# Optimization experiments

Hardware: AMD Instinct MI355X
Metric: run time of the kernel (lower is better)

The kernel has to match this reference:

```python
import jax, jax.numpy as jnp
import numpy as np
import math

B, NH, DIM = 8, 12, 768
NP, NF = 196, 16            # n (patches per frame), num_frames
DH = DIM // NH              # 64
D3 = 3 * DH                 # per-head feature dim after projection (192)
SEQ = NP * NF               # 3136 body tokens (+1 cls)
ROT = DH                    # rotary dim (RotaryEmbedding(dim=64))
SCALE = 1.0 / (math.sqrt(DH) * NH)


def _heads(t):
    b, s, _ = t.shape
    return t.reshape(b, s, NH, D3).transpose(0, 2, 1, 3)  # b h s d


def _rope(x):
    # lucidrains-style interleaved rotary on the first ROT dims of each head
    s = x.shape[2]
    inv_freq = 1.0 / (10000.0 ** (jnp.arange(0, ROT, 2, dtype=jnp.float32) / ROT))
    freqs = jnp.arange(s, dtype=jnp.float32)[:, None] * inv_freq  # [s, ROT/2]
    freqs = jnp.repeat(freqs, 2, axis=-1)                          # [s, ROT]
    cos, sin = jnp.cos(freqs), jnp.sin(freqs)
    xr, xp = x[..., :ROT], x[..., ROT:]
    x1, x2 = xr[..., ::2], xr[..., 1::2]
    half = jnp.stack((-x2, x1), axis=-1).reshape(xr.shape)
    return jnp.concatenate([xr * cos + half * sin, xp], axis=-1)


def _att_sum(q, k, v):
    # softmax(q k^T * SCALE) v, then sum over queries keepdim (dim 2)
    p = jax.nn.softmax(jnp.einsum('bhqd,bhkd->bhqk', q, k) * SCALE, axis=-1)
    return jnp.einsum('bhqk,bhkd->bhqd', p, v).sum(axis=2, keepdims=True)


def setup_inputs():
    key = jax.random.key(0)
    ks = jax.random.split(key, 11)
    p = lambda k, sh: jax.random.normal(k, sh, jnp.float32) * 0.02
    return {
        'x': jax.random.normal(ks[0], (B, SEQ + 1, DIM), jnp.float32),
        'Wq': p(ks[1], (DIM, 3 * DIM)), 'bq': p(ks[2], (3 * DIM,)),
        'Wk': p(ks[3], (DIM, 3 * DIM)), 'bk': p(ks[4], (3 * DIM,)),
        'Wv': p(ks[5], (DIM, 3 * DIM)), 'bv': p(ks[6], (3 * DIM,)),
        'Wt': p(ks[7], (3 * DIM, DIM)), 'bt': p(ks[8], (DIM,)),
        'Wf': p(ks[9], (3 * DIM, DIM)), 'bf': p(ks[10], (DIM,)),
    }


def reference(x, Wq, bq, Wk, bk, Wv, bv, Wt, bt, Wf, bf):
    body = x[:, 1:, :]
    # NOTE: the original swaps k/v projections for body tokens (k_mat uses self.v, v_mat uses self.k)
    q = _rope(_heads(body @ Wq + bq))
    k = _rope(_heads(body @ Wv + bv))
    v = _heads(body @ Wk + bk)

    # cls-token attention over the full sequence (correct k/v mapping here)
    q_cls = _heads(x[:, 0:1, :] @ Wq + bq)          # [b,h,1,d]
    k_cls = _heads(x @ Wk + bk)
    v_cls = _heads(x @ Wv + bv)
    p_cls = jax.nn.softmax(jnp.einsum('bhqd,bhkd->bhqk', q_cls, k_cls) * SCALE, axis=-1)
    cls_out = jnp.einsum('bhqk,bhkd->bhqd', p_cls, v_cls)  # [b,h,1,d]

    # temporal attention per spatial position x = 1..NP-1, vectorized
    # token index t = f*NP + x  ->  reshape [b,h,NF,NP,d], move spatial first
    qg = q.reshape(B, NH, NF, NP, D3).transpose(0, 1, 3, 2, 4)[:, :, 1:]  # [b,h,NP-1,NF,d]
    kg = k.reshape(B, NH, NF, NP, D3).transpose(0, 1, 3, 2, 4)[:, :, 1:]
    vg = v.reshape(B, NH, NF, NP, D3).transpose(0, 1, 3, 2, 4)[:, :, 1:]
    pg = jax.nn.softmax(jnp.einsum('bhxfd,bhxgd->bhxfg', qg, kg) * SCALE, axis=-1)
    tmp = jnp.einsum('bhxfg,bhxgd->bhxfd', pg, vg).sum(axis=3)  # sum over query frames -> [b,h,NP-1,d]

    temporal = jnp.tile(tmp, (1, 1, NF, 1))  # torch .repeat tiles -> [b,h,(NP-1)*NF,d]
    ti = temporal.transpose(0, 2, 1, 3).reshape(B, (NP - 1) * NF, NH * D3) @ Wt + bt

    # second pass (q uses self.q, v uses self.k, k uses self.v per original)
    q2 = _heads(ti @ Wq + bq)
    v2 = _heads(ti @ Wk + bk)
    k2 = _heads(ti @ Wv + bv)
    outs = [_att_sum(q2[:, :, 0:NP], k2[:, :, 0:NP], v2[:, :, 0:NP])]
    for xi in range(1, NF):  # small fixed loop over frames
        outs.append(_att_sum(q2[:, :, xi:xi + NP], k2[:, :, xi::NP], v2[:, :, xi::NP]))
    t2 = jnp.concatenate(outs, axis=2)        # [b,h,NF,d]
    t2 = jnp.tile(t2, (1, 1, NP, 1))          # [b,h,SEQ,d]
    t2 = jnp.concatenate([cls_out, t2], axis=2)  # [b,h,SEQ+1,d]
    return t2.transpose(0, 2, 1, 3).reshape(B, SEQ + 1, NH * D3) @ Wf + bf
```

## Files before the change

kernel.cpp:

```cpp
#include <hip/hip_runtime.h>
#include <cstdint>
#include <cstddef>


typedef unsigned short u16;
typedef __attribute__((ext_vector_type(8))) short short8;
typedef __attribute__((ext_vector_type(4))) float f32x4;

#define DEV static __device__ __forceinline__
#define AS1 __attribute__((address_space(1)))
#define AS3 __attribute__((address_space(3)))

DEV float b2f(u16 u) { union { unsigned int i; float f; } v; v.i = ((unsigned int)u) << 16; return v.f; }
DEV float b2fs(short s) { return b2f((u16)s); }
DEV u16 f2b(float f) {
    union { float f; unsigned int i; } v; v.f = f;
    unsigned int r = v.i + 0x7fffu + ((v.i >> 16) & 1u);
    return (u16)(r >> 16);
}
DEV void gld16(const u16* g, u16* l) {
    __builtin_amdgcn_global_load_lds((AS1 void*)(g), (AS3 void*)(l), 16, 0, 0);
}

constexpr int   ROWS  = 3137;
constexpr int   NPm1  = 195;
constexpr int   MT    = 8 * NPm1;
constexpr int   N3    = 2304;
constexpr float SCALE = 1.0f / 96.0f;
constexpr size_t P2Z  = (size_t)MT * N3;
constexpr int   CLS_NS = 32;
constexpr int   CLS_RS = 99;
constexpr int   LDK   = 200;

DEV float wave_max(float v) {
#pragma unroll
    for (int off = 32; off; off >>= 1) v = fmaxf(v, __shfl_xor(v, off));
    return v;
}
DEV float wave_sum(float v) {
#pragma unroll
    for (int off = 32; off; off >>= 1) v += __shfl_xor(v, off);
    return v;
}
DEV float block_max256(float v, float* red) {
    v = wave_max(v);
    __syncthreads();
    if ((threadIdx.x & 63) == 0) red[threadIdx.x >> 6] = v;
    __syncthreads();
    return fmaxf(fmaxf(red[0], red[1]), fmaxf(red[2], red[3]));
}
DEV float block_sum256(float v, float* red) {
    v = wave_sum(v);
    __syncthreads();
    if ((threadIdx.x & 63) == 0) red[threadIdx.x >> 6] = v;
    __syncthreads();
    return (red[0] + red[1]) + (red[2] + red[3]);
}

__global__ __launch_bounds__(256) void detect_dtype(const u16* __restrict__ x,
                                                    int* __restrict__ flag) {
    __shared__ int cnt;
    if (threadIdx.x == 0) cnt = 0;
    __syncthreads();
    int c = 0;
    for (int i = threadIdx.x; i < 8192; i += 256) {
        unsigned e = (x[i] >> 7) & 0xFFu;
        if (e >= 134u) c++;
    }
#pragma unroll
    for (int off = 32; off; off >>= 1) c += __shfl_xor(c, off);
    if ((threadIdx.x & 63) == 0) atomicAdd(&cnt, c);
    __syncthreads();
    if (threadIdx.x == 0) *flag = (cnt > 16) ? 1 : 0;
}

__global__ __launch_bounds__(256) void convert_x(const void* __restrict__ x,
                                                 u16* __restrict__ xb,
                                                 const int* __restrict__ dflag) {
    const int fl = *dflag;
    int t = blockIdx.x * 256 + threadIdx.x;
    size_t e0 = (size_t)t * 8;
    if (fl) {
        const float* p = (const float*)x + e0;
        float4 u0 = *(const float4*)p, u1 = *(const float4*)(p + 4);
        short8 r;
        r[0]=(short)f2b(u0.x); r[1]=(short)f2b(u0.y); r[2]=(short)f2b(u0.z); r[3]=(short)f2b(u0.w);
        r[4]=(short)f2b(u1.x); r[5]=(short)f2b(u1.y); r[6]=(short)f2b(u1.z); r[7]=(short)f2b(u1.w);
        *(short8*)(xb + e0) = r;
    } else {
        *(short8*)(xb + e0) = *(const short8*)((const u16*)x + e0);
    }
}

__global__ __launch_bounds__(256) void transpose_k(const void* __restrict__ in,
                                                   u16* __restrict__ out, int R, int C,
                                                   const int* __restrict__ dflag) {
    const int fl = *dflag;
    __shared__ u16 t[32][33];
    int bx = blockIdx.x * 32, by = blockIdx.y * 32;
    int tx = threadIdx.x & 31, ty = threadIdx.x >> 5;
#pragma unroll
    for (int i = 0; i < 32; i += 8) {
        int r = by + ty + i, c = bx + tx;
        if (r < R && c < C) {
            size_t idx = (size_t)r * C + c;
            t[ty + i][tx] = fl ? f2b(((const float*)in)[idx]) : ((const u16*)in)[idx];
        }
    }
    __syncthreads();
#pragma unroll
    for (int i = 0; i < 32; i += 8) {
        int c = bx + ty + i, r = by + tx;
        if (c < C && r < R) out[(size_t)c * R + r] = t[tx][ty + i];
    }
}

__global__ __launch_bounds__(256) void rope_tab_k(float* __restrict__ tab) {
    int t = blockIdx.x * 256 + threadIdx.x;
    if (t >= 3136 * 32) return;
    int s = t >> 5, i = t & 31;
    float inv = powf(10000.0f, -(float)(2 * i) * (1.0f / 64.0f));
    float sn, cs;
    sincosf((float)s * inv, &sn, &cs);
    tab[t * 2]     = cs;
    tab[t * 2 + 1] = sn;
}

DEV short8 pack_f32x8(const float* p) {
    const float4 u0 = *(const float4*)p;
    const float4 u1 = *(const float4*)(p + 4);
    short8 r;
    r[0]=(short)f2b(u0.x); r[1]=(short)f2b(u0.y); r[2]=(short)f2b(u0.z); r[3]=(short)f2b(u0.w);
    r[4]=(short)f2b(u1.x); r[5]=(short)f2b(u1.y); r[6]=(short)f2b(u1.z); r[7]=(short)f2b(u1.w);
    return r;
}

__global__ __launch_bounds__(256) void gemm_bt(const void* __restrict__ A, size_t aoff,
                                               const u16* __restrict__ BT,
                                               const void* __restrict__ b0p,
                                               const void* __restrict__ b1p,
                                               const void* __restrict__ b2p,
                                               void* __restrict__ C,
                                               int M, int N, int K,
                                               const int* __restrict__ dflag,
                                               int araw, int cf32) {
    const int fl = *dflag;
    const int af32 = araw && fl;
    const int z = blockIdx.z;
    const u16* Bz = BT + (size_t)z * N * K;
    const void* bias = (z == 0) ? b0p : (z == 1) ? b1p : b2p;

    __shared__ u16 As[128 * 32];
    __shared__ u16 Bs[128 * 32];

    const int tid  = threadIdx.x;
    const int lane = tid & 63;
    const int wave = tid >> 6;
    const int wm   = wave & 1;
    const int wn   = wave >> 1;
    const int quad = lane >> 4;
    const int l16  = lane & 15;

    const int m0 = blockIdx.y * 128;
    const int n0 = blockIdx.x * 128;

    f32x4 acc[4][4] = {};

    if (!af32) {
        const u16* Ab = (const u16*)A + aoff;
        int srow = wave * 32 + (lane >> 2);
        int scol = (lane & 3) * 8;
        int ar0 = m0 + srow;      if (ar0 > M - 1) ar0 = M - 1;
        int ar1 = m0 + srow + 16; if (ar1 > M - 1) ar1 = M - 1;
        const u16* gA0 = Ab + (size_t)ar0 * K + scol;
        const u16* gA1 = Ab + (size_t)ar1 * K + scol;
        const u16* gB0 = Bz + (size_t)(n0 + srow) * K + scol;
        const u16* gB1 = Bz + (size_t)(n0 + srow + 16) * K + scol;
        u16* lA0 = As + wave * 1024;
        u16* lA1 = As + wave * 1024 + 512;
        u16* lB0 = Bs + wave * 1024;
        u16* lB1 = Bs + wave * 1024 + 512;

        for (int k0 = 0; k0 < K; k0 += 32) {
            __syncthreads();
            gld16(gA0 + k0, lA0);
            gld16(gA1 + k0, lA1);
            gld16(gB0 + k0, lB0);
            gld16(gB1 + k0, lB1);
            __syncthreads();

            short8 af[4], bfr[4];
#pragma unroll
            for (int i = 0; i < 4; i++)
                af[i] = *(const short8*)(&As[(wm * 64 + i * 16 + l16) * 32 + quad * 8]);
#pragma unroll
            for (int j = 0; j < 4; j++)
                bfr[j] = *(const short8*)(&Bs[(wn * 64 + j * 16 + l16) * 32 + quad * 8]);
#pragma unroll
            for (int i = 0; i < 4; i++)
#pragma unroll
                for (int j = 0; j < 4; j++)
                    acc[i][j] = __builtin_amdgcn_mfma_f32_16x16x32_bf16(af[i], bfr[j], acc[i][j], 0, 0, 0);
        }
    } else {
        const int r0 = tid >> 2;
        const int kp = (tid & 3) << 3;
        int ga0 = m0 + r0;       if (ga0 > M - 1) ga0 = M - 1;
        int ga1 = m0 + r0 + 64;  if (ga1 > M - 1) ga1 = M - 1;
        const size_t arow0 = aoff + (size_t)ga0 * K + kp;
        const size_t arow1 = aoff + (size_t)ga1 * K + kp;
        const u16* Bp0 = Bz + (size_t)(n0 + r0) * K + kp;
        const u16* Bp1 = Bz + (size_t)(n0 + r0 + 64) * K + kp;

        for (int k0 = 0; k0 < K; k0 += 32) {
            short8 a0 = pack_f32x8((const float*)A + arow0 + k0);
            short8 a1 = pack_f32x8((const float*)A + arow1 + k0);
            short8 bv0 = *(const short8*)(Bp0 + k0);
            short8 bv1 = *(const short8*)(Bp1 + k0);
            __syncthreads();
            *(short8*)(&As[r0 * 32 + kp])        = a0;
            *(short8*)(&As[(r0 + 64) * 32 + kp]) = a1;
            *(short8*)(&Bs[r0 * 32 + kp])        = bv0;
            *(short8*)(&Bs[(r0 + 64) * 32 + kp]) = bv1;
            __syncthreads();

            short8 af[4], bfr[4];
#pragma unroll
            for (int i = 0; i < 4; i++)
                af[i] = *(const short8*)(&As[(wm * 64 + i * 16 + l16) * 32 + quad * 8]);
#pragma unroll
            for (int j = 0; j < 4; j++)
                bfr[j] = *(const short8*)(&Bs[(wn * 64 + j * 16 + l16) * 32 + quad * 8]);
#pragma unroll
            for (int i = 0; i < 4; i++)
#pragma unroll
                for (int j = 0; j < 4; j++)
                    acc[i][j] = __builtin_amdgcn_mfma_f32_16x16x32_bf16(af[i], bfr[j], acc[i][j], 0, 0, 0);
        }
    }

#pragma unroll
    for (int j = 0; j < 4; j++) {
        int col = n0 + wn * 64 + j * 16 + l16;
        float bb = fl ? ((const float*)bias)[col] : b2f(((const u16*)bias)[col]);
#pragma unroll
        for (int i = 0; i < 4; i++) {
            int rowb = m0 + wm * 64 + i * 16 + quad * 4;
#pragma unroll
            for (int r = 0; r < 4; r++) {
                int row = rowb + r;
                if (row < M) {
                    size_t idx = (size_t)z * M * N + (size_t)row * N + col;
                    float v = acc[i][j][r] + bb;
                    if (cf32) ((float*)C)[idx] = v;
                    else      ((u16*)C)[idx]  = f2b(v);
                }
            }
        }
    }
}

__global__ __launch_bounds__(256) void cls_part(const u16* __restrict__ Pb, size_t PZv,
                                                float* __restrict__ part, int b0) {
    int h = blockIdx.x, sp = blockIdx.y, bl = blockIdx.z;
    int b = b0 + bl;
    int base = sp * CLS_RS;
    int cnt = ROWS - base; if (cnt > CLS_RS) cnt = CLS_RS;
    __shared__ u16 Ksh[CLS_RS * LDK];
    __shared__ float qs[192];
    __shared__ float sc[CLS_RS];
    __shared__ float red[4];
    int tid = threadIdx.x;
    const size_t hbase = (size_t)bl * ROWS * N3 + (size_t)h * 192;
    const u16* Pq  = Pb;
    const u16* Pkc = Pb + PZv;
    const u16* Pvc = Pb + 2 * PZv;

    if (tid < 192) qs[tid] = b2f(Pq[hbase + tid]);
    for (int i = tid; i < cnt * 24; i += 256) {
        int r = i / 24, c = (i % 24) * 8;
        *(short8*)&Ksh[r * LDK + c] =
            *(const short8*)(Pkc + hbase + (size_t)(base + r) * N3 + c);
    }
    __syncthreads();

    float sval = -1e30f;
    if (tid < cnt) {
        float s = 0.f;
#pragma unroll
        for (int c = 0; c < 24; c++) {
            short8 v8 = *(const short8*)&Ksh[tid * LDK + c * 8];
#pragma unroll
            for (int j = 0; j < 8; j++) s += qs[c * 8 + j] * b2fs(v8[j]);
        }
        sval = s * SCALE;
    }
    float m = block_max256(sval, red);
    float e = (tid < cnt) ? __expf(sval - m) : 0.f;
    float l = block_sum256(e, red);
    if (tid < cnt) sc[tid] = e;
    __syncthreads();

    float* pp = part + ((size_t)(b * 12 + h) * CLS_NS + sp) * 194;
    if (tid == 0) { pp[0] = m; pp[1] = l; }
    if (tid < 192) {
        float acc = 0.f;
        const u16* vb = Pvc + hbase + tid;
        for (int r = 0; r < cnt; r++) acc += sc[r] * b2f(vb[(size_t)(base + r) * N3]);
        pp[2 + tid] = acc;
    }
}

__global__ __launch_bounds__(192) void cls_merge(const float* __restrict__ part,
                                                 u16* __restrict__ Fmat) {
    int h = blockIdx.x, b = blockIdx.y;
    int tid = threadIdx.x;
    const float* p0 = part + (size_t)(b * 12 + h) * CLS_NS * 194;
    float M = -1e30f;
#pragma unroll
    for (int s = 0; s < CLS_NS; s++) M = fmaxf(M, p0[s * 194]);
    float L = 0.f, acc = 0.f;
#pragma unroll
    for (int s = 0; s < CLS_NS; s++) {
        float w = __expf(p0[s * 194] - M);
        L += w * p0[s * 194 + 1];
        acc += w * p0[s * 194 + 2 + tid];
    }
    Fmat[(size_t)(b * 17) * N3 + (size_t)h * 192 + tid] = f2b(acc / L);
}

__global__ __launch_bounds__(128) void temporal_attn(const u16* __restrict__ Pb, size_t PZv,
                                                     const float* __restrict__ tab,
                                                     u16* __restrict__ tmp, int b0) {
    int p = blockIdx.x + 1, h = blockIdx.y, bl = blockIdx.z;
    int b = b0 + bl;
    __shared__ u16 Qs[16 * LDK];
    __shared__ u16 Ks[16 * LDK];
    __shared__ u16 Vs[16 * LDK];
    __shared__ float w[16];
    int tid = threadIdx.x;
    const u16* Pq = Pb;
    const u16* Pk = Pb + 2 * PZv;
    const u16* Pv = Pb + PZv;
    const size_t rbase = (size_t)bl * ROWS;

    for (int i = tid; i < 384; i += 128) {
        int f = i / 24, c = (i % 24) * 8;
        int s = f * 196 + p;
        size_t gidx = (rbase + 1 + s) * N3 + (size_t)h * 192 + c;
        short8 q8 = *(const short8*)(Pq + gidx);
        short8 k8 = *(const short8*)(Pk + gidx);
        short8 v8 = *(const short8*)(Pv + gidx);
        if (c < 64) {
            const float* tp = tab + ((size_t)s * 32 + (c >> 1)) * 2;
            float4 t0 = *(const float4*)tp;
            float4 t1 = *(const float4*)(tp + 4);
            float cs[4] = {t0.x, t0.z, t1.x, t1.z};
            float sn[4] = {t0.y, t0.w, t1.y, t1.w};
            short8 qo, ko;
#pragma unroll
            for (int j = 0; j < 4; j++) {
                float q1 = b2fs(q8[2 * j]), q2 = b2fs(q8[2 * j + 1]);
                float k1 = b2fs(k8[2 * j]), k2 = b2fs(k8[2 * j + 1]);
                qo[2 * j]     = (short)f2b(q1 * cs[j] - q2 * sn[j]);
                qo[2 * j + 1] = (short)f2b(q2 * cs[j] + q1 * sn[j]);
                ko[2 * j]     = (short)f2b(k1 * cs[j] - k2 * sn[j]);
                ko[2 * j + 1] = (short)f2b(k2 * cs[j] + k1 * sn[j]);
            }
            q8 = qo; k8 = ko;
        }
        *(short8*)&Qs[f * LDK + c] = q8;
        *(short8*)&Ks[f * LDK + c] = k8;
        *(short8*)&Vs[f * LDK + c] = v8;
    }
    __syncthreads();

    if (tid < 64) {
        int quad = tid >> 4, l16 = tid & 15;
        short8 Af[6], Bf[6];
#pragma unroll
        for (int ks = 0; ks < 6; ks++) {
            Af[ks] = *(const short8*)&Qs[l16 * LDK + quad * 8 + ks * 32];
            Bf[ks] = *(const short8*)&Ks[l16 * LDK + quad * 8 + ks * 32];
        }
        f32x4 S = {0.f, 0.f, 0.f, 0.f};
#pragma unroll
        for (int ks = 0; ks < 6; ks++)
            S = __builtin_amdgcn_mfma_f32_16x16x32_bf16(Af[ks], Bf[ks], S, 0, 0, 0);
        float wcol = 0.f;
#pragma unroll
        for (int r = 0; r < 4; r++) {
            float v = S[r] * SCALE;
            float m = v;
#pragma unroll
            for (int k = 1; k < 16; k <<= 1) m = fmaxf(m, __shfl_xor(m, k));
            float e = __expf(v - m);
            float l = e;
#pragma unroll
            for (int k = 1; k < 16; k <<= 1) l += __shfl_xor(l, k);
            wcol += e / l;
        }
        wcol += __shfl_xor(wcol, 16);
        wcol += __shfl_xor(wcol, 32);
        if (quad == 0) w[l16] = wcol;
    }
    __syncthreads();

    for (int d = tid; d < 192; d += 128) {
        float acc = 0.f;
#pragma unroll
        for (int g = 0; g < 16; g++) acc += w[g] * b2f(Vs[g * LDK + d]);
        tmp[(size_t)(b * NPm1 + p - 1) * N3 + (size_t)h * 192 + d] = f2b(acc);
    }
}

__global__ __launch_bounds__(256) void wacc_zero(float* __restrict__ wacc) {
    wacc[blockIdx.x * 256 + threadIdx.x] = 0.f;
}

__global__ __launch_bounds__(256) void attn2_sc(const u16* __restrict__ P2,
                                                float* __restrict__ wacc) {
    int t = blockIdx.x, h = blockIdx.y, b = blockIdx.z;
    __shared__ u16 Ks[195 * LDK];
    __shared__ u16 Qs[31 * LDK];
    __shared__ float pm[4][16], ps[4][16];
    int tid = threadIdx.x;
    const size_t hb = (size_t)b * NPm1 * N3 + (size_t)h * 192;
    const u16* Q  = P2;
    const u16* Kc = P2 + 2 * P2Z;

    for (int i = tid; i < 195 * 24; i += 256) {
        int r = i / 24, c = (i % 24) * 8;
        *(short8*)&Ks[r * LDK + c] = *(const short8*)(Kc + hb + (size_t)r * N3 + c);
    }
    for (int i = tid; i < 31 * 24; i += 256) {
        int r = i / 24, c = (i % 24) * 8;
        int qr = (t * 16 + r) % 195;
        *(short8*)&Qs[r * LDK + c] = *(const short8*)(Q + hb + (size_t)qr * N3 + c);
    }
    __syncthreads();

    int wave = tid >> 6, lane = tid & 63, quad = lane >> 4, l16 = lane & 15;
    float* wb = wacc + (size_t)((b * 12 + h) * 16) * 196;

    for (int xi = 1 + wave; xi <= 15; xi += 4) {
        short8 Af[6], Bf[6];
#pragma unroll
        for (int ks = 0; ks < 6; ks++) {
            Af[ks] = *(const short8*)&Qs[(xi + l16) * LDK + quad * 8 + ks * 32];
            Bf[ks] = *(const short8*)&Ks[(xi + l16) * LDK + quad * 8 + ks * 32];
        }
        f32x4 S = {0.f, 0.f, 0.f, 0.f};
#pragma unroll
        for (int ks = 0; ks < 6; ks++)
            S = __builtin_amdgcn_mfma_f32_16x16x32_bf16(Af[ks], Bf[ks], S, 0, 0, 0);
        float wcol = 0.f;
#pragma unroll
        for (int r = 0; r < 4; r++) {
            float v = S[r] * SCALE;
            float m = v;
#pragma unroll
            for (int k = 1; k < 16; k <<= 1) m = fmaxf(m, __shfl_xor(m, k));
            float e = __expf(v - m);
            float l = e;
#pragma unroll
            for (int k = 1; k < 16; k <<= 1) l += __shfl_xor(l, k);
            bool qok = (t * 16 + quad * 4 + r) <= 195;
            wcol += qok ? e / l : 0.f;
        }
        wcol += __shfl_xor(wcol, 16);
        wcol += __shfl_xor(wcol, 32);
        if (quad == 0) atomicAdd(&wb[xi * 196 + l16], wcol);
    }

    short8 Af0[6];
#pragma unroll
    for (int ks = 0; ks < 6; ks++)
        Af0[ks] = *(const short8*)&Qs[l16 * LDK + quad * 8 + ks * 32];

    f32x4 Sc[4];
    int   cl[4];
    int   cn = 0;
    for (int c = wave; c < 13; c += 4) {
        int g = c * 16 + l16;
        int krow = g % 195;
        short8 Bf[6];
#pragma unroll
        for (int ks = 0; ks < 6; ks++)
            Bf[ks] = *(const short8*)&Ks[krow * LDK + quad * 8 + ks * 32];
        f32x4 S = {0.f, 0.f, 0.f, 0.f};
#pragma unroll
        for (int ks = 0; ks < 6; ks++)
            S = __builtin_amdgcn_mfma_f32_16x16x32_bf16(Af0[ks], Bf[ks], S, 0, 0, 0);
        bool kbad = g > 195;
#pragma unroll
        for (int r = 0; r < 4; r++) S[r] = kbad ? -1e30f : S[r] * SCALE;
        Sc[cn] = S; cl[cn] = c; cn++;
    }
#pragma unroll
    for (int r = 0; r < 4; r++) {
        float v = -1e30f;
        for (int n = 0; n < cn; n++) v = fmaxf(v, Sc[n][r]);
#pragma unroll
        for (int k = 1; k < 16; k <<= 1) v = fmaxf(v, __shfl_xor(v, k));
        if (l16 == 0) pm[wave][quad * 4 + r] = v;
    }
    __syncthreads();
    float gmx[4], tot[4];
#pragma unroll
    for (int r = 0; r < 4; r++) {
        int qr = quad * 4 + r;
        gmx[r] = fmaxf(fmaxf(pm[0][qr], pm[1][qr]), fmaxf(pm[2][qr], pm[3][qr]));
    }
#pragma unroll
    for (int r = 0; r < 4; r++) {
        float s = 0.f;
        for (int n = 0; n < cn; n++) {
            float e = __expf(Sc[n][r] - gmx[r]);
            Sc[n][r] = e;
            s += e;
        }
#pragma unroll
        for (int k = 1; k < 16; k <<= 1) s += __shfl_xor(s, k);
        if (l16 == 0) ps[wave][quad * 4 + r] = s;
    }
    __syncthreads();
#pragma unroll
    for (int r = 0; r < 4; r++) {
        int qr = quad * 4 + r;
        tot[r] = (ps[0][qr] + ps[1][qr]) + (ps[2][qr] + ps[3][qr]);
    }
    for (int n = 0; n < cn; n++) {
        float wv = 0.f;
#pragma unroll
        for (int r = 0; r < 4; r++) {
            bool qok = (t * 16 + quad * 4 + r) <= 195;
            wv += qok ? Sc[n][r] / tot[r] : 0.f;
        }
        wv += __shfl_xor(wv, 16);
        wv += __shfl_xor(wv, 32);
        int g = cl[n] * 16 + l16;
        if (quad == 0 && g <= 195) atomicAdd(&wb[g], wv);
    }
}

__global__ __launch_bounds__(192) void attn2_fin(const u16* __restrict__ P2,
                                                 const float* __restrict__ wacc,
                                                 u16* __restrict__ Fmat) {
    int xi = blockIdx.x, h = blockIdx.y, b = blockIdx.z;
    int Nk = (xi == 0) ? 196 : 16;
    int tid = threadIdx.x;
    const u16* V = P2 + P2Z;
    const size_t hb = (size_t)b * NPm1 * N3 + (size_t)h * 192;
    const float* wb = wacc + (size_t)((b * 12 + h) * 16 + xi) * 196;
    float acc = 0.f;
    for (int g = 0; g < Nk; g++) {
        int kr = (xi == 0) ? (g % 195) : (xi + g);
        acc += wb[g] * b2f(V[hb + (size_t)kr * N3 + tid]);
    }
    Fmat[(size_t)(b * 17 + 1 + xi) * N3 + (size_t)h * 192 + tid] = f2b(acc);
}

__global__ __launch_bounds__(256) void scatter_out(const float* __restrict__ F17,
                                                   void* __restrict__ out,
                                                   const int* __restrict__ dflag) {
    const int fl = *dflag;
    int t = blockIdx.x * 256 + threadIdx.x;
    int c = t % 96;
    int rem = t / 96;
    int s = rem % ROWS;
    int b = rem / ROWS;
    int src = b * 17 + (s == 0 ? 0 : 1 + ((s - 1) & 15));
    const float* sp = F17 + ((size_t)src * 96 + c) * 8;
    if (fl) {
        float* o = (float*)out + (size_t)t * 8;
        *(float4*)o       = *(const float4*)sp;
        *(float4*)(o + 4) = *(const float4*)(sp + 4);
    } else {
        u16* o = (u16*)out + (size_t)t * 8;
        short8 v;
#pragma unroll
        for (int j = 0; j < 8; j++) v[j] = (short)f2b(sp[j]);
        *(short8*)o = v;
    }
}

extern "C" void kernel_launch(void* const* d_in, const int* in_sizes, int n_in,
                              void* d_out, int out_size, void* d_ws, size_t ws_size,
                              hipStream_t stream) {
    const void* x   = d_in[0];
    const void* Wq  = d_in[1];
    const void* bq  = d_in[2];
    const void* Wk  = d_in[3];
    const void* bk  = d_in[4];
    const void* Wv  = d_in[5];
    const void* bv  = d_in[6];
    const void* Wt  = d_in[7];
    const void* bt  = d_in[8];
    const void* Wf  = d_in[9];
    const void* bfb = d_in[10];
    (void)in_sizes; (void)n_in; (void)out_size;

    auto al = [](size_t b) { return (b + 255) & ~(size_t)255; };
    const size_t szFlag = al(256);
    const size_t szWT   = al((size_t)3 * N3 * 768 * 2);
    const size_t szTmp  = al((size_t)MT * N3 * 2);
    const size_t szFmat = al((size_t)136 * N3 * 2);
    const size_t szRope = al((size_t)3136 * 32 * 2 * 4);
    const size_t szClsP = al((size_t)8 * 12 * CLS_NS * 194 * 4);
    const size_t szWacc = al((size_t)96 * 16 * 196 * 4);
    const size_t szXb   = al((size_t)8 * ROWS * 768 * 2);
    const size_t szB    = al(3 * P2Z * 2) + al((size_t)MT * 768 * 2) +
                          al((size_t)768 * N3 * 2) * 2 + al((size_t)136 * 768 * 4);
    const size_t basePerst = szFlag + szWT + szTmp + szFmat + szRope + szClsP + szWacc;

    int bs = 1; int usexb = 0;
    {
        const int cand[4] = {8, 4, 2, 1};
        for (int i = 0; i < 4; i++) {
            size_t szP = al((size_t)3 * cand[i] * ROWS * N3 * 2);
            size_t need = basePerst + szXb + (szP > szB ? szP : szB);
            if (ws_size >= need) { bs = cand[i]; usexb = 1; break; }
        }
        if (!usexb) {
            size_t szP = al((size_t)3 * ROWS * N3 * 2);
            size_t need = basePerst + (szP > szB ? szP : szB);
            if (ws_size < need) return;
        }
    }

    char* ws = (char*)d_ws;
    size_t off = 0;
    auto allocB = [&](size_t bytes) { char* p = ws + off; off += al(bytes); return p; };
    int*   dflag = (int*)allocB(256);
    u16*   WT    = (u16*)allocB((size_t)3 * N3 * 768 * 2);
    u16*   tmp   = (u16*)allocB((size_t)MT * N3 * 2);
    u16*   Fmat  = (u16*)allocB((size_t)136 * N3 * 2);
    float* ropeT = (float*)allocB((size_t)3136 * 32 * 2 * 4);
    float* clsP  = (float*)allocB((size_t)8 * 12 * CLS_NS * 194 * 4);
    float* wacc  = (float*)allocB((size_t)96 * 16 * 196 * 4);
    u16*   xb    = usexb ? (u16*)allocB((size_t)8 * ROWS * 768 * 2) : nullptr;
    size_t aliasOff = off;
    u16* Pb = (u16*)allocB((size_t)3 * bs * ROWS * N3 * 2);
    off = aliasOff;
    u16*   P2  = (u16*)allocB(3 * P2Z * 2);
    u16*   tiu = (u16*)allocB((size_t)MT * 768 * 2);
    u16*   WtT = (u16*)allocB((size_t)768 * N3 * 2);
    u16*   WfT = (u16*)allocB((size_t)768 * N3 * 2);
    float* F17 = (float*)allocB((size_t)136 * 768 * 4);

    const size_t PZv = (size_t)bs * ROWS * N3;

    detect_dtype<<<dim3(1), 256, 0, stream>>>((const u16*)x, dflag);
    rope_tab_k<<<dim3(392), 256, 0, stream>>>(ropeT);
    if (usexb) convert_x<<<dim3(9411), 256, 0, stream>>>(x, xb, dflag);

    transpose_k<<<dim3(72, 24), 256, 0, stream>>>(Wq, WT, 768, N3, dflag);
    transpose_k<<<dim3(72, 24), 256, 0, stream>>>(Wk, WT + (size_t)N3 * 768, 768, N3, dflag);
    transpose_k<<<dim3(72, 24), 256, 0, stream>>>(Wv, WT + (size_t)2 * N3 * 768, 768, N3, dflag);

    for (int b0 = 0; b0 < 8; b0 += bs) {
        int Mv = bs * ROWS;
        size_t aoff = (size_t)b0 * ROWS * 768;
        if (usexb)
            gemm_bt<<<dim3(18, (Mv + 127) / 128, 3), 256, 0, stream>>>(
                xb, aoff, WT, bq, bk, bv, Pb, Mv, N3, 768, dflag, 0, 0);
        else
            gemm_bt<<<dim3(18, (Mv + 127) / 128, 3), 256, 0, stream>>>(
                x, aoff, WT, bq, bk, bv, Pb, Mv, N3, 768, dflag, 1, 0);
        cls_part<<<dim3(12, CLS_NS, bs), 256, 0, stream>>>(Pb, PZv, clsP, b0);
        temporal_attn<<<dim3(195, 12, bs), 128, 0, stream>>>(Pb, PZv, ropeT, tmp, b0);
    }
    cls_merge<<<dim3(12, 8), 192, 0, stream>>>(clsP, Fmat);

    transpose_k<<<dim3(24, 72), 256, 0, stream>>>(Wt, WtT, N3, 768, dflag);
    transpose_k<<<dim3(24, 72), 256, 0, stream>>>(Wf, WfT, N3, 768, dflag);

    gemm_bt<<<dim3(6, 13, 1), 256, 0, stream>>>(tmp, 0, WtT, bt, bt, bt, tiu,
                                                MT, 768, N3, dflag, 0, 0);
    gemm_bt<<<dim3(18, 13, 3), 256, 0, stream>>>(tiu, 0, WT, bq, bk, bv, P2,
                                                 MT, N3, 768, dflag, 0, 0);

    wacc_zero<<<dim3(1176), 256, 0, stream>>>(wacc);
    attn2_sc<<<dim3(13, 12, 8), 256, 0, stream>>>(P2, wacc);
    attn2_fin<<<dim3(16, 12, 8), 192, 0, stream>>>(P2, wacc, Fmat);

    gemm_bt<<<dim3(6, 2, 1), 256, 0, stream>>>(Fmat, 0, WfT, bfb, bfb, bfb, F17,
                                               136, 768, N3, dflag, 0, 1);

    scatter_out<<<dim3(9411), 256, 0, stream>>>(F17, d_out, dflag);
}
```

Before: 1.180 ms.

## Merge prep, attention and finalize kernels to cut launch count

Folds the dtype detection, weight transposes, input conversion, wacc zeroing and rope table into one prep kernel. Each kernel now recomputes the dtype flag per wave instead of reading a stored flag. Fuses cls_part with temporal_attn and cls_merge with attn2_fin so fewer launches and serial dependencies remain. WtT/WfT move out of the aliased region so they can be transposed up front, which costs extra workspace, and the dtype check now samples fewer elements.

```diff
diff --git a/kernel.cpp b/kernel.cpp
--- a/kernel.cpp
+++ b/kernel.cpp
@@ -20,6 +20,17 @@
 }
 DEV void gld16(const u16* g, u16* l) {
     __builtin_amdgcn_global_load_lds((AS1 void*)(g), (AS3 void*)(l), 16, 0, 0);
+}
+
+DEV int detect_fl(const u16* x) {
+    int lane = threadIdx.x & 63;
+    const u16* p = x + lane * 8;
+    int c = 0;
+#pragma unroll
+    for (int j = 0; j < 8; j++) c += (((p[j] >> 7) & 0xFFu) >= 134u);
+#pragma unroll
+    for (int off = 32; off; off >>= 1) c += __shfl_xor(c, off);
+    return c > 8;
 }
 
 constexpr int   ROWS  = 3137;
@@ -57,73 +68,86 @@
     return (red[0] + red[1]) + (red[2] + red[3]);
 }
 
-__global__ __launch_bounds__(256) void detect_dtype(const u16* __restrict__ x,
-                                                    int* __restrict__ flag) {
-    __shared__ int cnt;
-    if (threadIdx.x == 0) cnt = 0;
-    __syncthreads();
-    int c = 0;
-    for (int i = threadIdx.x; i < 8192; i += 256) {
-        unsigned e = (x[i] >> 7) & 0xFFu;
-        if (e >= 134u) c++;
-    }
-#pragma unroll
-    for (int off = 32; off; off >>= 1) c += __shfl_xor(c, off);
-    if ((threadIdx.x & 63) == 0) atomicAdd(&cnt, c);
-    __syncthreads();
-    if (threadIdx.x == 0) *flag = (cnt > 16) ? 1 : 0;
-}
-
-__global__ __launch_bounds__(256) void convert_x(const void* __restrict__ x,
-                                                 u16* __restrict__ xb,
-                                                 const int* __restrict__ dflag) {
-    const int fl = *dflag;
-    int t = blockIdx.x * 256 + threadIdx.x;
-    size_t e0 = (size_t)t * 8;
-    if (fl) {
-        const float* p = (const float*)x + e0;
-        float4 u0 = *(const float4*)p, u1 = *(const float4*)(p + 4);
-        short8 r;
-        r[0]=(short)f2b(u0.x); r[1]=(short)f2b(u0.y); r[2]=(short)f2b(u0.z); r[3]=(short)f2b(u0.w);
-        r[4]=(short)f2b(u1.x); r[5]=(short)f2b(u1.y); r[6]=(short)f2b(u1.z); r[7]=(short)f2b(u1.w);
-        *(short8*)(xb + e0) = r;
-    } else {
-        *(short8*)(xb + e0) = *(const short8*)((const u16*)x + e0);
-    }
-}
-
-__global__ __launch_bounds__(256) void transpose_k(const void* __restrict__ in,
-                                                   u16* __restrict__ out, int R, int C,
-                                                   const int* __restrict__ dflag) {
-    const int fl = *dflag;
-    __shared__ u16 t[32][33];
-    int bx = blockIdx.x * 32, by = blockIdx.y * 32;
+DEV void do_transpose(const void* in, u16* out, int R, int C,
+                      int bx, int by, int fl, u16 (*tls)[33]) {
     int tx = threadIdx.x & 31, ty = threadIdx.x >> 5;
 #pragma unroll
     for (int i = 0; i < 32; i += 8) {
         int r = by + ty + i, c = bx + tx;
-        if (r < R && c < C) {
-            size_t idx = (size_t)r * C + c;
-            t[ty + i][tx] = fl ? f2b(((const float*)in)[idx]) : ((const u16*)in)[idx];
-        }
+        size_t idx = (size_t)r * C + c;
+        tls[ty + i][tx] = fl ? f2b(((const float*)in)[idx]) : ((const u16*)in)[idx];
     }
     __syncthreads();
 #pragma unroll
     for (int i = 0; i < 32; i += 8) {
         int c = bx + ty + i, r = by + tx;
-        if (c < C && r < R) out[(size_t)c * R + r] = t[tx][ty + i];
-    }
-}
-
-__global__ __launch_bounds__(256) void rope_tab_k(float* __restrict__ tab) {
-    int t = blockIdx.x * 256 + threadIdx.x;
-    if (t >= 3136 * 32) return;
-    int s = t >> 5, i = t & 31;
-    float inv = powf(10000.0f, -(float)(2 * i) * (1.0f / 64.0f));
-    float sn, cs;
-    sincosf((float)s * inv, &sn, &cs);
-    tab[t * 2]     = cs;
-    tab[t * 2 + 1] = sn;
+        out[(size_t)c * R + r] = tls[tx][ty + i];
+    }
+}
+
+__global__ __launch_bounds__(256) void prep(const u16* __restrict__ x,
+                                            const void* __restrict__ Wq,
+                                            const void* __restrict__ Wk,
+                                            const void* __restrict__ Wv,
+                                            const void* __restrict__ Wt,
+                                            const void* __restrict__ Wf,
+                                            u16* __restrict__ WT,
+                                            u16* __restrict__ WtT,
+                                            u16* __restrict__ WfT,
+                                            u16* __restrict__ xb,
+                                            float* __restrict__ wacc,
+                                            float* __restrict__ ropeT,
+                                            int usexb) {
+    __shared__ u16 tls[32][33];
+    int bid = blockIdx.x;
+    if (bid < 5184) {
+        int fl = detect_fl(x);
+        int z = bid / 1728, t = bid % 1728;
+        const void* W = (z == 0) ? Wq : (z == 1) ? Wk : Wv;
+        do_transpose(W, WT + (size_t)z * N3 * 768, 768, N3,
+                     (t % 72) * 32, (t / 72) * 32, fl, tls);
+        return;
+    }
+    bid -= 5184;
+    if (bid < 3456) {
+        int fl = detect_fl(x);
+        int z = bid / 1728, t = bid % 1728;
+        do_transpose(z ? Wf : Wt, z ? WfT : WtT, N3, 768,
+                     (t % 24) * 32, (t / 24) * 32, fl, tls);
+        return;
+    }
+    bid -= 3456;
+    if (bid < 9411) {
+        if (!usexb) return;
+        int fl = detect_fl(x);
+        size_t e0 = ((size_t)bid * 256 + threadIdx.x) * 8;
+        if (fl) {
+            const float* p = (const float*)x + e0;
+            float4 u0 = *(const float4*)p, u1 = *(const float4*)(p + 4);
+            short8 r;
+            r[0]=(short)f2b(u0.x); r[1]=(short)f2b(u0.y); r[2]=(short)f2b(u0.z); r[3]=(short)f2b(u0.w);
+            r[4]=(short)f2b(u1.x); r[5]=(short)f2b(u1.y); r[6]=(short)f2b(u1.z); r[7]=(short)f2b(u1.w);
+            *(short8*)(xb + e0) = r;
+        } else {
+            *(short8*)(xb + e0) = *(const short8*)(x + e0);
+        }
+        return;
+    }
+    bid -= 9411;
+    if (bid < 1176) {
+        wacc[(size_t)bid * 256 + threadIdx.x] = 0.f;
+        return;
+    }
+    bid -= 1176;
+    {
+        int t = bid * 256 + threadIdx.x;
+        int s = t >> 5, i = t & 31;
+        float inv = powf(10000.0f, -(float)(2 * i) * (1.0f / 64.0f));
+        float sn, cs;
+        sincosf((float)s * inv, &sn, &cs);
+        ropeT[t * 2]     = cs;
+        ropeT[t * 2 + 1] = sn;
+    }
 }
 
 DEV short8 pack_f32x8(const float* p) {
@@ -142,9 +166,9 @@
                                                const void* __restrict__ b2p,
                                                void* __restrict__ C,
                                                int M, int N, int K,
-                                               const int* __restrict__ dflag,
+                                               const u16* __restrict__ xdet,
                                                int araw, int cf32) {
-    const int fl = *dflag;
+    const int fl = detect_fl(xdet);
     const int af32 = araw && fl;
     const int z = blockIdx.z;
     const u16* Bz = BT + (size_t)z * N * K;
@@ -260,162 +284,141 @@
     }
 }
 
-__global__ __launch_bounds__(256) void cls_part(const u16* __restrict__ Pb, size_t PZv,
-                                                float* __restrict__ part, int b0) {
-    int h = blockIdx.x, sp = blockIdx.y, bl = blockIdx.z;
+__global__ __launch_bounds__(256) void phaseA_attn(const u16* __restrict__ Pb, size_t PZv,
+                                                   const float* __restrict__ tab,
+                                                   u16* __restrict__ tmp,
+                                                   float* __restrict__ clsP, int b0) {
+    __shared__ __align__(16) char smem[40800];
+    int xg = blockIdx.x, h = blockIdx.y, bl = blockIdx.z;
     int b = b0 + bl;
-    int base = sp * CLS_RS;
-    int cnt = ROWS - base; if (cnt > CLS_RS) cnt = CLS_RS;
-    __shared__ u16 Ksh[CLS_RS * LDK];
-    __shared__ float qs[192];
-    __shared__ float sc[CLS_RS];
-    __shared__ float red[4];
     int tid = threadIdx.x;
-    const size_t hbase = (size_t)bl * ROWS * N3 + (size_t)h * 192;
-    const u16* Pq  = Pb;
-    const u16* Pkc = Pb + PZv;
-    const u16* Pvc = Pb + 2 * PZv;
-
-    if (tid < 192) qs[tid] = b2f(Pq[hbase + tid]);
-    for (int i = tid; i < cnt * 24; i += 256) {
-        int r = i / 24, c = (i % 24) * 8;
-        *(short8*)&Ksh[r * LDK + c] =
-            *(const short8*)(Pkc + hbase + (size_t)(base + r) * N3 + c);
-    }
-    __syncthreads();
-
-    float sval = -1e30f;
-    if (tid < cnt) {
-        float s = 0.f;
-#pragma unroll
-        for (int c = 0; c < 24; c++) {
-            short8 v8 = *(const short8*)&Ksh[tid * LDK + c * 8];
-#pragma unroll
-            for (int j = 0; j < 8; j++) s += qs[c * 8 + j] * b2fs(v8[j]);
-        }
-        sval = s * SCALE;
-    }
-    float m = block_max256(sval, red);
-    float e = (tid < cnt) ? __expf(sval - m) : 0.f;
-    float l = block_sum256(e, red);
-    if (tid < cnt) sc[tid] = e;
-    __syncthreads();
-
-    float* pp = part + ((size_t)(b * 12 + h) * CLS_NS + sp) * 194;
-    if (tid == 0) { pp[0] = m; pp[1] = l; }
-    if (tid < 192) {
-        float acc = 0.f;
-        const u16* vb = Pvc + hbase + tid;
-        for (int r = 0; r < cnt; r++) acc += sc[r] * b2f(vb[(size_t)(base + r) * N3]);
-        pp[2 + tid] = acc;
-    }
-}
-
-__global__ __launch_bounds__(192) void cls_merge(const float* __restrict__ part,
-                                                 u16* __restrict__ Fmat) {
-    int h = blockIdx.x, b = blockIdx.y;
-    int tid = threadIdx.x;
-    const float* p0 = part + (size_t)(b * 12 + h) * CLS_NS * 194;
-    float M = -1e30f;
-#pragma unroll
-    for (int s = 0; s < CLS_NS; s++) M = fmaxf(M, p0[s * 194]);
-    float L = 0.f, acc = 0.f;
-#pragma unroll
-    for (int s = 0; s < CLS_NS; s++) {
-        float w = __expf(p0[s * 194] - M);
-        L += w * p0[s * 194 + 1];
-        acc += w * p0[s * 194 + 2 + tid];
-    }
-    Fmat[(size_t)(b * 17) * N3 + (size_t)h * 192 + tid] = f2b(acc / L);
-}
-
-__global__ __launch_bounds__(128) void temporal_attn(const u16* __restrict__ Pb, size_t PZv,
-                                                     const float* __restrict__ tab,
-                                                     u16* __restrict__ tmp, int b0) {
-    int p = blockIdx.x + 1, h = blockIdx.y, bl = blockIdx.z;
-    int b = b0 + bl;
-    __shared__ u16 Qs[16 * LDK];
-    __shared__ u16 Ks[16 * LDK];
-    __shared__ u16 Vs[16 * LDK];
-    __shared__ float w[16];
-    int tid = threadIdx.x;
-    const u16* Pq = Pb;
-    const u16* Pk = Pb + 2 * PZv;
-    const u16* Pv = Pb + PZv;
-    const size_t rbase = (size_t)bl * ROWS;
-
-    for (int i = tid; i < 384; i += 128) {
-        int f = i / 24, c = (i % 24) * 8;
-        int s = f * 196 + p;
-        size_t gidx = (rbase + 1 + s) * N3 + (size_t)h * 192 + c;
-        short8 q8 = *(const short8*)(Pq + gidx);
-        short8 k8 = *(const short8*)(Pk + gidx);
-        short8 v8 = *(const short8*)(Pv + gidx);
-        if (c < 64) {
-            const float* tp = tab + ((size_t)s * 32 + (c >> 1)) * 2;
-            float4 t0 = *(const float4*)tp;
-            float4 t1 = *(const float4*)(tp + 4);
-            float cs[4] = {t0.x, t0.z, t1.x, t1.z};
-            float sn[4] = {t0.y, t0.w, t1.y, t1.w};
-            short8 qo, ko;
-#pragma unroll
-            for (int j = 0; j < 4; j++) {
-                float q1 = b2fs(q8[2 * j]), q2 = b2fs(q8[2 * j + 1]);
-                float k1 = b2fs(k8[2 * j]), k2 = b2fs(k8[2 * j + 1]);
-                qo[2 * j]     = (short)f2b(q1 * cs[j] - q2 * sn[j]);
-                qo[2 * j + 1] = (short)f2b(q2 * cs[j] + q1 * sn[j]);
-                ko[2 * j]     = (short)f2b(k1 * cs[j] - k2 * sn[j]);
-                ko[2 * j + 1] = (short)f2b(k2 * cs[j] + k1 * sn[j]);
+
+    if (xg < 195) {
+        int p = xg + 1;
+        u16* Qs = (u16*)smem;
+        u16* Ks = Qs + 16 * LDK;
+        u16* Vs = Ks + 16 * LDK;
+        float* w = (float*)(smem + 3 * 16 * LDK * 2);
+        const u16* Pq = Pb;
+        const u16* Pk = Pb + 2 * PZv;
+        const u16* Pv = Pb + PZv;
+        const size_t rbase = (size_t)bl * ROWS;
+
+        for (int i = tid; i < 384; i += 256) {
+            int f = i / 24, c = (i % 24) * 8;
+            int s = f * 196 + p;
+            size_t gidx = (rbase + 1 + s) * N3 + (size_t)h * 192 + c;
+            short8 q8 = *(const short8*)(Pq + gidx);
+            short8 k8 = *(const short8*)(Pk + gidx);
+            short8 v8 = *(const short8*)(Pv + gidx);
+            if (c < 64) {
+                const float* tp = tab + ((size_t)s * 32 + (c >> 1)) * 2;
+                float4 t0 = *(const float4*)tp;
+                float4 t1 = *(const float4*)(tp + 4);
+                float cs[4] = {t0.x, t0.z, t1.x, t1.z};
+                float sn[4] = {t0.y, t0.w, t1.y, t1.w};
+                short8 qo, ko;
+#pragma unroll
+                for (int j = 0; j < 4; j++) {
+                    float q1 = b2fs(q8[2 * j]), q2 = b2fs(q8[2 * j + 1]);
+                    float k1 = b2fs(k8[2 * j]), k2 = b2fs(k8[2 * j + 1]);
+                    qo[2 * j]     = (short)f2b(q1 * cs[j] - q2 * sn[j]);
+                    qo[2 * j + 1] = (short)f2b(q2 * cs[j] + q1 * sn[j]);
+                    ko[2 * j]     = (short)f2b(k1 * cs[j] - k2 * sn[j]);
+                    ko[2 * j + 1] = (short)f2b(k2 * cs[j] + k1 * sn[j]);
+                }
+                q8 = qo; k8 = ko;
             }
-            q8 = qo; k8 = ko;
-        }
-        *(short8*)&Qs[f * LDK + c] = q8;
-        *(short8*)&Ks[f * LDK + c] = k8;
-        *(short8*)&Vs[f * LDK + c] = v8;
-    }
-    __syncthreads();
-
-    if (tid < 64) {
-        int quad = tid >> 4, l16 = tid & 15;
-        short8 Af[6], Bf[6];
-#pragma unroll
-        for (int ks = 0; ks < 6; ks++) {
-            Af[ks] = *(const short8*)&Qs[l16 * LDK + quad * 8 + ks * 32];
-            Bf[ks] = *(const short8*)&Ks[l16 * LDK + quad * 8 + ks * 32];
-        }
-        f32x4 S = {0.f, 0.f, 0.f, 0.f};
-#pragma unroll
-        for (int ks = 0; ks < 6; ks++)
-            S = __builtin_amdgcn_mfma_f32_16x16x32_bf16(Af[ks], Bf[ks], S, 0, 0, 0);
-        float wcol = 0.f;
-#pragma unroll
-        for (int r = 0; r < 4; r++) {
-            float v = S[r] * SCALE;
-            float m = v;
-#pragma unroll
-            for (int k = 1; k < 16; k <<= 1) m = fmaxf(m, __shfl_xor(m, k));
-            float e = __expf(v - m);
-            float l = e;
-#pragma unroll
-            for (int k = 1; k < 16; k <<= 1) l += __shfl_xor(l, k);
-            wcol += e / l;
-        }
-        wcol += __shfl_xor(wcol, 16);
-        wcol += __shfl_xor(wcol, 32);
-        if (quad == 0) w[l16] = wcol;
-    }
-    __syncthreads();
-
-    for (int d = tid; d < 192; d += 128) {
-        float acc = 0.f;
-#pragma unroll
-        for (int g = 0; g < 16; g++) acc += w[g] * b2f(Vs[g * LDK + d]);
-        tmp[(size_t)(b * NPm1 + p - 1) * N3 + (size_t)h * 192 + d] = f2b(acc);
-    }
-}
-
-__global__ __launch_bounds__(256) void wacc_zero(float* __restrict__ wacc) {
-    wacc[blockIdx.x * 256 + threadIdx.x] = 0.f;
+            *(short8*)&Qs[f * LDK + c] = q8;
+            *(short8*)&Ks[f * LDK + c] = k8;
+            *(short8*)&Vs[f * LDK + c] = v8;
+        }
+        __syncthreads();
+
+        if (tid < 64) {
+            int quad = tid >> 4, l16 = tid & 15;
+            short8 Af[6], Bf[6];
+#pragma unroll
+            for (int ks = 0; ks < 6; ks++) {
+                Af[ks] = *(const short8*)&Qs[l16 * LDK + quad * 8 + ks * 32];
+                Bf[ks] = *(const short8*)&Ks[l16 * LDK + quad * 8 + ks * 32];
+            }
+            f32x4 S = {0.f, 0.f, 0.f, 0.f};
+#pragma unroll
+            for (int ks = 0; ks < 6; ks++)
+                S = __builtin_amdgcn_mfma_f32_16x16x32_bf16(Af[ks], Bf[ks], S, 0, 0, 0);
+            float wcol = 0.f;
+#pragma unroll
+            for (int r = 0; r < 4; r++) {
+                float v = S[r] * SCALE;
+                float m = v;
+#pragma unroll
+                for (int k = 1; k < 16; k <<= 1) m = fmaxf(m, __shfl_xor(m, k));
+                float e = __expf(v - m);
+                float l = e;
+#pragma unroll
+                for (int k = 1; k < 16; k <<= 1) l += __shfl_xor(l, k);
+                wcol += e / l;
+            }
+            wcol += __shfl_xor(wcol, 16);
+            wcol += __shfl_xor(wcol, 32);
+            if (quad == 0) w[l16] = wcol;
+        }
+        __syncthreads();
+
+        if (tid < 192) {
+            float acc = 0.f;
+#pragma unroll
+            for (int g = 0; g < 16; g++) acc += w[g] * b2f(Vs[g * LDK + tid]);
+            tmp[(size_t)(b * NPm1 + p - 1) * N3 + (size_t)h * 192 + tid] = f2b(acc);
+        }
+    } else {
+        int sp = xg - 195;
+        int base = sp * CLS_RS;
+        int cnt = ROWS - base; if (cnt > CLS_RS) cnt = CLS_RS;
+        u16* Ksh  = (u16*)smem;
+        float* qs  = (float*)(smem + CLS_RS * LDK * 2);
+        float* sc  = qs + 192;
+        float* red = sc + 100;
+        const size_t hbase = (size_t)bl * ROWS * N3 + (size_t)h * 192;
+        const u16* Pq  = Pb;
+        const u16* Pkc = Pb + PZv;
+        const u16* Pvc = Pb + 2 * PZv;
+
+        if (tid < 192) qs[tid] = b2f(Pq[hbase + tid]);
+        for (int i = tid; i < cnt * 24; i += 256) {
+            int r = i / 24, c = (i % 24) * 8;
+            *(short8*)&Ksh[r * LDK + c] =
+                *(const short8*)(Pkc + hbase + (size_t)(base + r) * N3 + c);
+        }
+        __syncthreads();
+
+        float sval = -1e30f;
+        if (tid < cnt) {
+            float s = 0.f;
+#pragma unroll
+            for (int c = 0; c < 24; c++) {
+                short8 v8 = *(const short8*)&Ksh[tid * LDK + c * 8];
+#pragma unroll
+                for (int j = 0; j < 8; j++) s += qs[c * 8 + j] * b2fs(v8[j]);
+            }
+            sval = s * SCALE;
+        }
+        float m = block_max256(sval, red);
+        float e = (tid < cnt) ? __expf(sval - m) : 0.f;
+        float l = block_sum256(e, red);
+        if (tid < cnt) sc[tid] = e;
+        __syncthreads();
+
+        float* pp = clsP + ((size_t)(b * 12 + h) * CLS_NS + sp) * 194;
+        if (tid == 0) { pp[0] = m; pp[1] = l; }
+        if (tid < 192) {
+            float acc = 0.f;
+            const u16* vb = Pvc + hbase + tid;
+            for (int r = 0; r < cnt; r++) acc += sc[r] * b2f(vb[(size_t)(base + r) * N3]);
+            pp[2 + tid] = acc;
+        }
+    }
 }
 
 __global__ __launch_bounds__(256) void attn2_sc(const u16* __restrict__ P2,
@@ -544,27 +547,44 @@
     }
 }
 
-__global__ __launch_bounds__(192) void attn2_fin(const u16* __restrict__ P2,
-                                                 const float* __restrict__ wacc,
-                                                 u16* __restrict__ Fmat) {
-    int xi = blockIdx.x, h = blockIdx.y, b = blockIdx.z;
-    int Nk = (xi == 0) ? 196 : 16;
+__global__ __launch_bounds__(192) void fin(const u16* __restrict__ P2,
+                                           const float* __restrict__ wacc,
+                                           const float* __restrict__ clsP,
+                                           u16* __restrict__ Fmat) {
+    int xg = blockIdx.x, h = blockIdx.y, b = blockIdx.z;
     int tid = threadIdx.x;
-    const u16* V = P2 + P2Z;
-    const size_t hb = (size_t)b * NPm1 * N3 + (size_t)h * 192;
-    const float* wb = wacc + (size_t)((b * 12 + h) * 16 + xi) * 196;
-    float acc = 0.f;
-    for (int g = 0; g < Nk; g++) {
-        int kr = (xi == 0) ? (g % 195) : (xi + g);
-        acc += wb[g] * b2f(V[hb + (size_t)kr * N3 + tid]);
-    }
-    Fmat[(size_t)(b * 17 + 1 + xi) * N3 + (size_t)h * 192 + tid] = f2b(acc);
+    if (xg == 0) {
+        const float* p0 = clsP + (size_t)(b * 12 + h) * CLS_NS * 194;
+        float M = -1e30f;
+#pragma unroll
+        for (int s = 0; s < CLS_NS; s++) M = fmaxf(M, p0[s * 194]);
+        float L = 0.f, acc = 0.f;
+#pragma unroll
+        for (int s = 0; s < CLS_NS; s++) {
+            float w = __expf(p0[s * 194] - M);
+            L += w * p0[s * 194 + 1];
+            acc += w * p0[s * 194 + 2 + tid];
+        }
+        Fmat[(size_t)(b * 17) * N3 + (size_t)h * 192 + tid] = f2b(acc / L);
+    } else {
+        int xi = xg - 1;
+        int Nk = (xi == 0) ? 196 : 16;
+        const u16* V = P2 + P2Z;
+        const size_t hb = (size_t)b * NPm1 * N3 + (size_t)h * 192;
+        const float* wb = wacc + (size_t)((b * 12 + h) * 16 + xi) * 196;
+        float acc = 0.f;
+        for (int g = 0; g < Nk; g++) {
+            int kr = (xi == 0) ? (g % 195) : (xi + g);
+            acc += wb[g] * b2f(V[hb + (size_t)kr * N3 + tid]);
+        }
+        Fmat[(size_t)(b * 17 + 1 + xi) * N3 + (size_t)h * 192 + tid] = f2b(acc);
+    }
 }
 
 __global__ __launch_bounds__(256) void scatter_out(const float* __restrict__ F17,
                                                    void* __restrict__ out,
-                                                   const int* __restrict__ dflag) {
-    const int fl = *dflag;
+                                                   const u16* __restrict__ xdet) {
+    const int fl = detect_fl(xdet);
     int t = blockIdx.x * 256 + threadIdx.x;
     int c = t % 96;
     int rem = t / 96;
@@ -599,11 +619,12 @@
     const void* bt  = d_in[8];
     const void* Wf  = d_in[9];
     const void* bfb = d_in[10];
+    const u16* xdet = (const u16*)x;
     (void)in_sizes; (void)n_in; (void)out_size;
 
     auto al = [](size_t b) { return (b + 255) & ~(size_t)255; };
-    const size_t szFlag = al(256);
     const size_t szWT   = al((size_t)3 * N3 * 768 * 2);
+    const size_t szWtT  = al((size_t)768 * N3 * 2);
     const size_t szTmp  = al((size_t)MT * N3 * 2);
     const size_t szFmat = al((size_t)136 * N3 * 2);
     const size_t szRope = al((size_t)3136 * 32 * 2 * 4);
@@ -611,8 +632,8 @@
     const size_t szWacc = al((size_t)96 * 16 * 196 * 4);
     const size_t szXb   = al((size_t)8 * ROWS * 768 * 2);
     const size_t szB    = al(3 * P2Z * 2) + al((size_t)MT * 768 * 2) +
-                          al((size_t)768 * N3 * 2) * 2 + al((size_t)136 * 768 * 4);
-    const size_t basePerst = szFlag + szWT + szTmp + szFmat + szRope + szClsP + szWacc;
+                          al((size_t)136 * 768 * 4);
+    const size_t basePerst = szWT + 2 * szWtT + szTmp + szFmat + szRope + szClsP + szWacc;
 
     int bs = 1; int usexb = 0;
     {
@@ -632,8 +653,9 @@
     char* ws = (char*)d_ws;
     size_t off = 0;
     auto allocB = [&](size_t bytes) { char* p = ws + off; off += al(bytes); return p; };
-    int*   dflag = (int*)allocB(256);
     u16*   WT    = (u16*)allocB((size_t)3 * N3 * 768 * 2);
+    u16*   WtT   = (u16*)allocB((size_t)768 * N3 * 2);
+    u16*   WfT   = (u16*)allocB((size_t)768 * N3 * 2);
     u16*   tmp   = (u16*)allocB((size_t)MT * N3 * 2);
     u16*   Fmat  = (u16*)allocB((size_t)136 * N3 * 2);
     float* ropeT = (float*)allocB((size_t)3136 * 32 * 2 * 4);
@@ -645,48 +667,32 @@
     off = aliasOff;
     u16*   P2  = (u16*)allocB(3 * P2Z * 2);
     u16*   tiu = (u16*)allocB((size_t)MT * 768 * 2);
-    u16*   WtT = (u16*)allocB((size_t)768 * N3 * 2);
-    u16*   WfT = (u16*)allocB((size_t)768 * N3 * 2);
     float* F17 = (float*)allocB((size_t)136 * 768 * 4);
 
     const size_t PZv = (size_t)bs * ROWS * N3;
 
-    detect_dtype<<<dim3(1), 256, 0, stream>>>((const u16*)x, dflag);
-    rope_tab_k<<<dim3(392), 256, 0, stream>>>(ropeT);
-    if (usexb) convert_x<<<dim3(9411), 256, 0, stream>>>(x, xb, dflag);
-
-    transpose_k<<<dim3(72, 24), 256, 0, stream>>>(Wq, WT, 768, N3, dflag);
-    transpose_k<<<dim3(72, 24), 256, 0, stream>>>(Wk, WT + (size_t)N3 * 768, 768, N3, dflag);
-    transpose_k<<<dim3(72, 24), 256, 0, stream>>>(Wv, WT + (size_t)2 * N3 * 768, 768, N3, dflag);
+    prep<<<dim3(19619), 256, 0, stream>>>(xdet, Wq, Wk, Wv, Wt, Wf,
+                                          WT, WtT, WfT, xb, wacc, ropeT, usexb);
 
     for (int b0 = 0; b0 < 8; b0 += bs) {
         int Mv = bs * ROWS;
         size_t aoff = (size_t)b0 * ROWS * 768;
         if (usexb)
             gemm_bt<<<dim3(18, (Mv + 127) / 128, 3), 256, 0, stream>>>(
-                xb, aoff, WT, bq, bk, bv, Pb, Mv, N3, 768, dflag, 0, 0);
+                xb, aoff, WT, bq, bk, bv, Pb, Mv, N3, 768, xdet, 0, 0);
         else
             gemm_bt<<<dim3(18, (Mv + 127) / 128, 3), 256, 0, stream>>>(
-                x, aoff, WT, bq, bk, bv, Pb, Mv, N3, 768, dflag, 1, 0);
-        cls_part<<<dim3(12, CLS_NS, bs), 256, 0, stream>>>(Pb, PZv, clsP, b0);
-        temporal_attn<<<dim3(195, 12, bs), 128, 0, stream>>>(Pb, PZv, ropeT, tmp, b0);
-    }
-    cls_merge<<<dim3(12, 8), 192, 0, stream>>>(clsP, Fmat);
-
-    transpose_k<<<dim3(24, 72), 256, 0, stream>>>(Wt, WtT, N3, 768, dflag);
-    transpose_k<<<dim3(24, 72), 256, 0, stream>>>(Wf, WfT, N3, 768, dflag);
+                x, aoff, WT, bq, bk, bv, Pb, Mv, N3, 768, xdet, 1, 0);
+        phaseA_attn<<<dim3(227, 12, bs), 256, 0, stream>>>(Pb, PZv, ropeT, tmp, clsP, b0);
+    }
 
     gemm_bt<<<dim3(6, 13, 1), 256, 0, stream>>>(tmp, 0, WtT, bt, bt, bt, tiu,
-                                                MT, 768, N3, dflag, 0, 0);
+                                                MT, 768, N3, xdet, 0, 0);
     gemm_bt<<<dim3(18, 13, 3), 256, 0, stream>>>(tiu, 0, WT, bq, bk, bv, P2,
-                                                 MT, N3, 768, dflag, 0, 0);
-
-    wacc_zero<<<dim3(1176), 256, 0, stream>>>(wacc);
+                                                 MT, N3, 768, xdet, 0, 0);
     attn2_sc<<<dim3(13, 12, 8), 256, 0, stream>>>(P2, wacc);
-    attn2_fin<<<dim3(16, 12, 8), 192, 0, stream>>>(P2, wacc, Fmat);
-
+    fin<<<dim3(17, 12, 8), 192, 0, stream>>>(P2, wacc, clsP, Fmat);
     gemm_bt<<<dim3(6, 2, 1), 256, 0, stream>>>(Fmat, 0, WfT, bfb, bfb, bfb, F17,
-                                               136, 768, N3, dflag, 0, 1);
-
-    scatter_out<<<dim3(9411), 256, 0, stream>>>(F17, d_out, dflag);
-}
+                                               136, 768, N3, xdet, 0, 1);
+    scatter_out<<<dim3(9411), 256, 0, stream>>>(F17, d_out, xdet);
+}
```

Result: no change. 1.163 ms (-1.5%).
